# Kernel tuning notes

Measured on AMD Instinct MI355X. Metric: run time of the kernel, lower is better.

Reference implementation:

```python
import jax, jax.numpy as jnp
import numpy as np

N_ATOMS = 200000   # total atoms across batch of molecules
N_BONDS = 400000   # total directed bonds
HSIZE   = 256      # mpn_size
MLP     = 512      # mlp_size
BS_OUT  = 5        # bond edit classes (bs_outdim)
N_MOLS  = 1000     # batch of molecules (len(atom_scope))


def _p(k, shape, scale):
    return jax.random.normal(k, shape, jnp.float32) * scale


def setup_inputs() -> dict:
    key = jax.random.key(0)
    ks = jax.random.split(key, 12)
    s_h = 1.0 / np.sqrt(HSIZE).astype(np.float32)
    s_2h = 1.0 / np.sqrt(2 * HSIZE).astype(np.float32)
    s_m = 1.0 / np.sqrt(MLP).astype(np.float32)
    return {
        'c_atom':  jax.random.normal(ks[0], (N_ATOMS, HSIZE), jnp.float32),
        'ha_prev': jax.random.normal(ks[1], (N_ATOMS, HSIZE), jnp.float32),
        'W_vv':    jnp.eye(HSIZE, dtype=jnp.float32),  # nn.init.eye_ in original
        'W_vc':    _p(ks[2], (HSIZE, HSIZE), s_h),
        'bond_W1': _p(ks[3], (2 * HSIZE, MLP), s_2h),
        'bond_b1': jnp.zeros((MLP,), jnp.float32),
        'bond_W2': _p(ks[4], (MLP, BS_OUT), s_m),
        'bond_b2': jnp.zeros((BS_OUT,), jnp.float32),
        'uni_W1':  _p(ks[5], (HSIZE, MLP), s_h),
        'uni_b1':  jnp.zeros((MLP,), jnp.float32),
        'uni_W2':  _p(ks[6], (MLP, 1), s_m),
        'uni_b2':  jnp.zeros((1,), jnp.float32),
        'done_W1': _p(ks[7], (HSIZE, MLP), s_h),
        'done_b1': jnp.zeros((MLP,), jnp.float32),
        'done_W2': _p(ks[8], (MLP, 1), s_m),
        'done_b2': jnp.zeros((1,), jnp.float32),
        'mol_id':     jax.random.randint(ks[9], (N_ATOMS,), 0, N_MOLS, jnp.int32),
        'bond_index': jax.random.randint(ks[10], (N_BONDS, 2), 0, N_ATOMS, jnp.int32),
    }


def _mlp(x, W1, b1, W2, b2):
    # build_mlp: Linear -> ReLU -> (dropout, off at eval) -> Linear
    return jax.nn.relu(x @ W1 + b1) @ W2 + b2


def reference(c_atom, ha_prev, W_vv, W_vc,
              bond_W1, bond_b1, bond_W2, bond_b2,
              uni_W1, uni_b1, uni_W2, uni_b2,
              done_W1, done_b1, done_W2, done_b2,
              mol_id, bond_index):
    # ha = relu(W_vv @ ha_prev + W_vc @ c_atom); ha[0] = 0 (padding atom)
    ha = jax.nn.relu(ha_prev @ W_vv + c_atom @ W_vc)
    ha = ha.at[0].set(0.0)
    # per-molecule pooling (replaces python loop over atom_scope)
    hm = jax.ops.segment_sum(ha, mol_id, num_segments=N_MOLS)  # [N_MOLS, H]
    # gather bond endpoint embeddings (index_select_ND)
    bond_in = jnp.concatenate([ha[bond_index[:, 0]], ha[bond_index[:, 1]]], axis=-1)  # [E, 2H]
    bond_logits = _mlp(bond_in, bond_W1, bond_b1, bond_W2, bond_b2)  # [E, BS_OUT]
    uni_logits = _mlp(ha, uni_W1, uni_b1, uni_W2, uni_b2)            # [N, 1]
    done_logits = _mlp(hm, done_W1, done_b1, done_W2, done_b2)       # [M, 1]
    # edit_logits in original is a ragged per-mol concat of these three;
    # return the dense flat concatenation (same values, fixed shape)
    return jnp.concatenate([bond_logits.ravel(), uni_logits.ravel(), done_logits.ravel()])
```

## Files before the change

### kernel.cpp

```cpp
#include <hip/hip_runtime.h>
#include <hip/hip_bf16.h>

typedef __attribute__((ext_vector_type(8))) short bf16x8;
typedef __attribute__((ext_vector_type(4))) float f32x4;

static __device__ __forceinline__ unsigned short f2bf(float f) {
    union { float f; unsigned u; } v; v.f = f;
    unsigned r = v.u + 0x7fffu + ((v.u >> 16) & 1u);
    return (unsigned short)(r >> 16);
}

#define GLOAD16(g, l) __builtin_amdgcn_global_load_lds( \
    (const __attribute__((address_space(1))) void*)(g), \
    (__attribute__((address_space(3))) void*)(l), 16, 0, 0)

__global__ __launch_bounds__(256) void conv_weights(
    const float* __restrict__ Wvv, const float* __restrict__ Wvc,
    const float* __restrict__ bW1, const float* __restrict__ uW1,
    unsigned short* __restrict__ WcT, unsigned short* __restrict__ bW1T,
    unsigned short* __restrict__ uW1T)
{
    int idx = blockIdx.x * 256 + threadIdx.x;
    if (idx < 131072) {
        int n = idx & 255, k = idx >> 8;
        float s = (k < 256) ? Wvv[k * 256 + n] : Wvc[(k - 256) * 256 + n];
        WcT[((k >> 3) * 256 + n) * 8 + (k & 7)] = f2bf(s);
    } else if (idx < 131072 + 262144) {
        int t = idx - 131072;
        int n = t & 511, k = t >> 9;
        bW1T[((k >> 3) * 512 + n) * 8 + (k & 7)] = f2bf(bW1[k * 512 + n]);
    } else if (idx < 131072 + 262144 + 131072) {
        int t = idx - 393216;
        int n = t & 511, k = t >> 9;
        uW1T[((k >> 3) * 512 + n) * 8 + (k & 7)] = f2bf(uW1[k * 512 + n]);
    }
}

__global__ __launch_bounds__(512, 4) void ha_kernel(
    const float* __restrict__ ha_prev, const float* __restrict__ c_atom,
    const unsigned short* __restrict__ WcT, const int* __restrict__ mol_id,
    unsigned short* __restrict__ haB, float* __restrict__ hm, int NA)
{
    __shared__ __align__(16) unsigned short As[2][128 * 64];

    const int tid = threadIdx.x;
    const int wv = tid >> 6, lane = tid & 63;
    const int wr = wv >> 2, wc = wv & 3;
    const int c15 = lane & 15, kq = lane >> 4;
    const int xm3 = (c15 & 7) << 3;
    const int m0 = blockIdx.x * 128;

    const int cr0 = tid >> 3, chc = tid & 7;
    const int cr1 = (512 + tid) >> 3;
    int row0 = m0 + cr0; if (row0 >= NA) row0 = NA - 1;
    int row1 = m0 + cr1; if (row1 >= NA) row1 = NA - 1;

    f32x4 v00, v01, v10, v11;
    #define HA_LOAD(ks) { \
        const float* src = ((ks) < 4) ? ha_prev : c_atom; \
        const int kb = ((ks) & 3) * 64 + chc * 8; \
        const float* s0 = src + (size_t)row0 * 256 + kb; \
        const float* s1 = src + (size_t)row1 * 256 + kb; \
        v00 = *(const f32x4*)s0; v01 = *(const f32x4*)(s0 + 4); \
        v10 = *(const f32x4*)s1; v11 = *(const f32x4*)(s1 + 4); }
    #define HA_WRITE(buf) { \
        bf16x8 p0, p1; \
        p0[0]=(short)f2bf(v00[0]); p0[1]=(short)f2bf(v00[1]); p0[2]=(short)f2bf(v00[2]); p0[3]=(short)f2bf(v00[3]); \
        p0[4]=(short)f2bf(v01[0]); p0[5]=(short)f2bf(v01[1]); p0[6]=(short)f2bf(v01[2]); p0[7]=(short)f2bf(v01[3]); \
        p1[0]=(short)f2bf(v10[0]); p1[1]=(short)f2bf(v10[1]); p1[2]=(short)f2bf(v10[2]); p1[3]=(short)f2bf(v10[3]); \
        p1[4]=(short)f2bf(v11[0]); p1[5]=(short)f2bf(v11[1]); p1[6]=(short)f2bf(v11[2]); p1[7]=(short)f2bf(v11[3]); \
        *(bf16x8*)&As[buf][cr0 * 64 + ((chc * 8) ^ ((cr0 & 7) << 3))] = p0; \
        *(bf16x8*)&As[buf][cr1 * 64 + ((chc * 8) ^ ((cr1 & 7) << 3))] = p1; }

    f32x4 acc[4][4];
#pragma unroll
    for (int m = 0; m < 4; ++m)
#pragma unroll
        for (int n = 0; n < 4; ++n) acc[m][n] = (f32x4){0.f, 0.f, 0.f, 0.f};

    HA_LOAD(0); HA_WRITE(0);
    __syncthreads();

    for (int ks = 0; ks < 8; ++ks) {
        if (ks < 7) HA_LOAD(ks + 1);
        const int buf = ks & 1;
#pragma unroll
        for (int kk = 0; kk < 2; ++kk) {
            bf16x8 aF[4], bF[4];
            const int plane = ks * 8 + kk * 4 + kq;
#pragma unroll
            for (int n = 0; n < 4; ++n)
                bF[n] = *(const bf16x8*)(WcT + ((size_t)plane * 256 + wc * 64 + n * 16 + c15) * 8);
#pragma unroll
            for (int m = 0; m < 4; ++m)
                aF[m] = *(const bf16x8*)&As[buf][(wr * 64 + m * 16 + c15) * 64 + ((kk * 32 + kq * 8) ^ xm3)];
#pragma unroll
            for (int m = 0; m < 4; ++m)
#pragma unroll
                for (int n = 0; n < 4; ++n)
                    acc[m][n] = __builtin_amdgcn_mfma_f32_16x16x32_bf16(aF[m], bF[n], acc[m][n], 0, 0, 0);
        }
        if (ks < 7) HA_WRITE((ks + 1) & 1);
        __syncthreads();
    }

#pragma unroll
    for (int m = 0; m < 4; ++m) {
#pragma unroll
        for (int reg = 0; reg < 4; ++reg) {
            int row = m0 + wr * 64 + m * 16 + kq * 4 + reg;
            if (row >= NA) continue;
            bool z = (row == 0);
            int mol = z ? 0 : mol_id[row];
#pragma unroll
            for (int n = 0; n < 4; ++n) {
                int col = wc * 64 + n * 16 + c15;
                float v = fmaxf(acc[m][n][reg], 0.f);
                if (z) v = 0.f;
                haB[(size_t)row * 256 + col] = f2bf(v);
                if (!z) atomicAdd(&hm[mol * 256 + col], v);
            }
        }
    }
}

__global__ __launch_bounds__(512, 4) void bond_kernel(
    const unsigned short* __restrict__ haB, const int* __restrict__ bidx,
    const unsigned short* __restrict__ bW1T, const float* __restrict__ b1,
    const float* __restrict__ W2, const float* __restrict__ b2,
    float* __restrict__ outB, int NB)
{
    __shared__ __align__(16) unsigned short As[64 * 512];
    __shared__ float obuf[64][5];

    const int tid = threadIdx.x;
    const int wv = tid >> 6, lane = tid & 63;
    const int c15 = lane & 15, kq = lane >> 4;
    const int b0 = blockIdx.x * 64;

    if (tid < 320) ((float*)obuf)[tid] = 0.f;

    const int ep = lane >> 5, sl = lane & 31;
    int eidx[8];
#pragma unroll
    for (int i = 0; i < 8; ++i) {
        int gb = b0 + wv * 8 + i; if (gb >= NB) gb = 0;
        eidx[i] = bidx[gb * 2 + ep];
    }
#pragma unroll
    for (int i = 0; i < 8; ++i) {
        int r = wv * 8 + i;
        GLOAD16(haB + (size_t)eidx[i] * 256 + (size_t)((sl ^ (r & 7)) * 8),
                As + r * 512);
    }
    __syncthreads();

    f32x4 acc[4][4];
#pragma unroll
    for (int m = 0; m < 4; ++m)
#pragma unroll
        for (int n = 0; n < 4; ++n) acc[m][n] = (f32x4){0.f, 0.f, 0.f, 0.f};

    for (int ks = 0; ks < 8; ++ks) {
#pragma unroll
        for (int kk = 0; kk < 2; ++kk) {
            bf16x8 aF[4], bF[4];
            const int plane = ks * 8 + kk * 4 + kq;
#pragma unroll
            for (int n = 0; n < 4; ++n)
                bF[n] = *(const bf16x8*)(bW1T + ((size_t)plane * 512 + wv * 64 + n * 16 + c15) * 8);
#pragma unroll
            for (int m = 0; m < 4; ++m) {
                int r = m * 16 + c15;
                int ch = (((ks & 3) * 8 + kk * 4 + kq) ^ (r & 7));
                aF[m] = *(const bf16x8*)&As[r * 512 + (ks >> 2) * 256 + ch * 8];
            }
#pragma unroll
            for (int m = 0; m < 4; ++m)
#pragma unroll
                for (int n = 0; n < 4; ++n)
                    acc[m][n] = __builtin_amdgcn_mfma_f32_16x16x32_bf16(aF[m], bF[n], acc[m][n], 0, 0, 0);
        }
    }

    float b1c[4], w2c[4][5];
#pragma unroll
    for (int n = 0; n < 4; ++n) {
        int col = wv * 64 + n * 16 + c15;
        b1c[n] = b1[col];
#pragma unroll
        for (int j = 0; j < 5; ++j) w2c[n][j] = W2[col * 5 + j];
    }
#pragma unroll
    for (int m = 0; m < 4; ++m) {
#pragma unroll
        for (int reg = 0; reg < 4; ++reg) {
            float s[5] = {0.f, 0.f, 0.f, 0.f, 0.f};
#pragma unroll
            for (int n = 0; n < 4; ++n) {
                float p = fmaxf(acc[m][n][reg] + b1c[n], 0.f);
#pragma unroll
                for (int j = 0; j < 5; ++j) s[j] += p * w2c[n][j];
            }
#pragma unroll
            for (int off = 1; off < 16; off <<= 1)
#pragma unroll
                for (int j = 0; j < 5; ++j) s[j] += __shfl_xor(s[j], off);
            if (c15 == 0) {
                int rl = m * 16 + kq * 4 + reg;
#pragma unroll
                for (int j = 0; j < 5; ++j) atomicAdd(&obuf[rl][j], s[j]);
            }
        }
    }
    __syncthreads();
    {
        int r = tid >> 3, j = tid & 7;
        if (j < 5) {
            int row = b0 + r;
            if (row < NB) outB[(size_t)row * 5 + j] = obuf[r][j] + b2[j];
        }
    }
}

__global__ __launch_bounds__(512, 4) void uni_kernel(
    const unsigned short* __restrict__ haB, const unsigned short* __restrict__ uW1T,
    const float* __restrict__ b1, const float* __restrict__ W2,
    const float* __restrict__ b2, float* __restrict__ outU, int NA)
{
    __shared__ __align__(16) unsigned short As[64 * 256];
    __shared__ float obuf[64];

    const int tid = threadIdx.x;
    const int wv = tid >> 6, lane = tid & 63;
    const int c15 = lane & 15, kq = lane >> 4;
    const int a0 = blockIdx.x * 64;

    if (tid < 64) obuf[tid] = 0.f;

    const int rr = lane >> 5, sl = lane & 31;
#pragma unroll
    for (int i = 0; i < 4; ++i) {
        int r = wv * 8 + i * 2 + rr;
        int ga = a0 + r; if (ga >= NA) ga = NA - 1;
        GLOAD16(haB + (size_t)ga * 256 + (size_t)((sl ^ (r & 7)) * 8),
                As + (wv * 8 + i * 2) * 256);
    }
    __syncthreads();

    f32x4 acc[4][4];
#pragma unroll
    for (int m = 0; m < 4; ++m)
#pragma unroll
        for (int n = 0; n < 4; ++n) acc[m][n] = (f32x4){0.f, 0.f, 0.f, 0.f};

    for (int ks = 0; ks < 4; ++ks) {
#pragma unroll
        for (int kk = 0; kk < 2; ++kk) {
            bf16x8 aF[4], bF[4];
            const int plane = ks * 8 + kk * 4 + kq;
#pragma unroll
            for (int n = 0; n < 4; ++n)
                bF[n] = *(const bf16x8*)(uW1T + ((size_t)plane * 512 + wv * 64 + n * 16 + c15) * 8);
#pragma unroll
            for (int m = 0; m < 4; ++m) {
                int r = m * 16 + c15;
                int ch = ((ks * 8 + kk * 4 + kq) ^ (r & 7));
                aF[m] = *(const bf16x8*)&As[r * 256 + ch * 8];
            }
#pragma unroll
            for (int m = 0; m < 4; ++m)
#pragma unroll
                for (int n = 0; n < 4; ++n)
                    acc[m][n] = __builtin_amdgcn_mfma_f32_16x16x32_bf16(aF[m], bF[n], acc[m][n], 0, 0, 0);
        }
    }

    float b1c[4], w2c[4];
#pragma unroll
    for (int n = 0; n < 4; ++n) {
        int col = wv * 64 + n * 16 + c15;
        b1c[n] = b1[col];
        w2c[n] = W2[col];
    }
#pragma unroll
    for (int m = 0; m < 4; ++m) {
#pragma unroll
        for (int reg = 0; reg < 4; ++reg) {
            float s = 0.f;
#pragma unroll
            for (int n = 0; n < 4; ++n)
                s += fmaxf(acc[m][n][reg] + b1c[n], 0.f) * w2c[n];
#pragma unroll
            for (int off = 1; off < 16; off <<= 1) s += __shfl_xor(s, off);
            if (c15 == 0) atomicAdd(&obuf[m * 16 + kq * 4 + reg], s);
        }
    }
    __syncthreads();
    if (tid < 64) {
        int row = a0 + tid;
        if (row < NA) outU[row] = obuf[tid] + b2[0];
    }
}

__global__ __launch_bounds__(256) void done_kernel(
    const float* __restrict__ hm, const float* __restrict__ W1,
    const float* __restrict__ b1, const float* __restrict__ W2,
    const float* __restrict__ b2, float* __restrict__ outD, int NM)
{
    __shared__ float rsh[4][256];
    __shared__ float red[4][4];
    const int tid = threadIdx.x;
    const int wv = tid >> 6, lane = tid & 63;
    const int mol0 = blockIdx.x * 4;
#pragma unroll
    for (int q = 0; q < 4; ++q)
        rsh[q][tid] = (mol0 + q < NM) ? hm[(size_t)(mol0 + q) * 256 + tid] : 0.f;
    __syncthreads();
    float h[4][2];
#pragma unroll
    for (int q = 0; q < 4; ++q) { h[q][0] = 0.f; h[q][1] = 0.f; }
    for (int k = 0; k < 256; ++k) {
        float w0 = W1[k * 512 + tid];
        float w1 = W1[k * 512 + tid + 256];
#pragma unroll
        for (int q = 0; q < 4; ++q) {
            h[q][0] += rsh[q][k] * w0;
            h[q][1] += rsh[q][k] * w1;
        }
    }
    float bb0 = b1[tid], bb1v = b1[tid + 256];
    float ww0 = W2[tid], ww1 = W2[tid + 256];
#pragma unroll
    for (int q = 0; q < 4; ++q) {
        float p = fmaxf(h[q][0] + bb0, 0.f) * ww0 + fmaxf(h[q][1] + bb1v, 0.f) * ww1;
#pragma unroll
        for (int off = 1; off < 64; off <<= 1) p += __shfl_xor(p, off);
        if (lane == 0) red[q][wv] = p;
    }
    __syncthreads();
    if (tid < 4 && mol0 + tid < NM)
        outD[mol0 + tid] = red[tid][0] + red[tid][1] + red[tid][2] + red[tid][3] + b2[0];
}

extern "C" void kernel_launch(void* const* d_in, const int* in_sizes, int n_in,
                              void* d_out, int out_size, void* d_ws, size_t ws_size,
                              hipStream_t stream)
{
    const float* c_atom  = (const float*)d_in[0];
    const float* ha_prev = (const float*)d_in[1];
    const float* W_vv    = (const float*)d_in[2];
    const float* W_vc    = (const float*)d_in[3];
    const float* bW1     = (const float*)d_in[4];
    const float* bb1     = (const float*)d_in[5];
    const float* bW2     = (const float*)d_in[6];
    const float* bb2     = (const float*)d_in[7];
    const float* uW1     = (const float*)d_in[8];
    const float* ub1     = (const float*)d_in[9];
    const float* uW2     = (const float*)d_in[10];
    const float* ub2     = (const float*)d_in[11];
    const float* dW1     = (const float*)d_in[12];
    const float* db1     = (const float*)d_in[13];
    const float* dW2     = (const float*)d_in[14];
    const float* db2     = (const float*)d_in[15];
    const int* mol_id    = (const int*)d_in[16];
    const int* bidx      = (const int*)d_in[17];

    const int H = 256, BS = 5;
    const int NA = in_sizes[0] / H;
    const int NB = in_sizes[17] / 2;
    const int NM = out_size - NB * BS - NA;

    float* out  = (float*)d_out;
    float* outB = out;
    float* outU = out + (size_t)NB * BS;
    float* outD = outU + NA;

    char* ws = (char*)d_ws;
    size_t off = 0;
    unsigned short* haB = (unsigned short*)(ws + off);
    off += (size_t)NA * H * 2;            off = (off + 255) & ~(size_t)255;
    float* hm = (float*)(ws + off);
    off += (size_t)NM * H * 4;            off = (off + 255) & ~(size_t)255;
    unsigned short* WcT = (unsigned short*)(ws + off);
    off += (size_t)131072 * 2;            off = (off + 255) & ~(size_t)255;
    unsigned short* bW1T = (unsigned short*)(ws + off);
    off += (size_t)262144 * 2;            off = (off + 255) & ~(size_t)255;
    unsigned short* uW1T = (unsigned short*)(ws + off);

    hipMemsetAsync(hm, 0, (size_t)NM * H * 4, stream);
    conv_weights<<<2048, 256, 0, stream>>>(W_vv, W_vc, bW1, uW1, WcT, bW1T, uW1T);
    ha_kernel<<<(NA + 127) / 128, 512, 0, stream>>>(ha_prev, c_atom, WcT, mol_id, haB, hm, NA);
    bond_kernel<<<(NB + 63) / 64, 512, 0, stream>>>(haB, bidx, bW1T, bb1, bW2, bb2, outB, NB);
    uni_kernel<<<(NA + 63) / 64, 512, 0, stream>>>(haB, uW1T, ub1, uW2, ub2, outU, NA);
    done_kernel<<<(NM + 3) / 4, 256, 0, stream>>>(hm, dW1, db1, dW2, db2, outD, NM);
}
```

Baseline: 633.3 us.

## Retile LDS A staging by K-blocks and double-buffer weight fragment loads

The bond and uni kernels now stage the gathered activation tile in LDS as 64-column K-blocks, with each wave loading one K-slab across all rows instead of whole rows. The MFMA loop is fully unrolled and prefetches the next step's weight fragments into a second register buffer while the current step computes. The intent is to hide global weight-load latency behind the MFMAs and to change the gather access pattern. The extra register buffer may reduce occupancy under the launch bound.

```diff
diff --git a/kernel.cpp b/kernel.cpp
--- a/kernel.cpp
+++ b/kernel.cpp
@@ -130,7 +130,7 @@
     const float* __restrict__ W2, const float* __restrict__ b2,
     float* __restrict__ outB, int NB)
 {
-    __shared__ __align__(16) unsigned short As[64 * 512];
+    __shared__ __align__(16) unsigned short As[8 * 64 * 64];
     __shared__ float obuf[64][5];
 
     const int tid = threadIdx.x;
@@ -140,18 +140,21 @@
 
     if (tid < 320) ((float*)obuf)[tid] = 0.f;
 
-    const int ep = lane >> 5, sl = lane & 31;
-    int eidx[8];
-#pragma unroll
-    for (int i = 0; i < 8; ++i) {
-        int gb = b0 + wv * 8 + i; if (gb >= NB) gb = 0;
-        eidx[i] = bidx[gb * 2 + ep];
-    }
-#pragma unroll
-    for (int i = 0; i < 8; ++i) {
-        int r = wv * 8 + i;
-        GLOAD16(haB + (size_t)eidx[i] * 256 + (size_t)((sl ^ (r & 7)) * 8),
-                As + r * 512);
+    {
+        const int ep = wv >> 2, koff = (wv & 3) * 64;
+        const int rsub = lane >> 3, csub = lane & 7;
+        int eidxs[8];
+#pragma unroll
+        for (int j = 0; j < 8; ++j) {
+            int gb = b0 + j * 8 + rsub; if (gb >= NB) gb = 0;
+            eidxs[j] = bidx[gb * 2 + ep];
+        }
+#pragma unroll
+        for (int j = 0; j < 8; ++j) {
+            int r = j * 8 + rsub;
+            GLOAD16(haB + (size_t)eidxs[j] * 256 + koff + (size_t)((csub ^ (r & 7)) * 8),
+                    As + wv * 4096 + j * 512);
+        }
     }
     __syncthreads();
 
@@ -161,26 +164,33 @@
 #pragma unroll
         for (int n = 0; n < 4; ++n) acc[m][n] = (f32x4){0.f, 0.f, 0.f, 0.f};
 
-    for (int ks = 0; ks < 8; ++ks) {
-#pragma unroll
-        for (int kk = 0; kk < 2; ++kk) {
-            bf16x8 aF[4], bF[4];
-            const int plane = ks * 8 + kk * 4 + kq;
-#pragma unroll
-            for (int n = 0; n < 4; ++n)
-                bF[n] = *(const bf16x8*)(bW1T + ((size_t)plane * 512 + wv * 64 + n * 16 + c15) * 8);
-#pragma unroll
-            for (int m = 0; m < 4; ++m) {
-                int r = m * 16 + c15;
-                int ch = (((ks & 3) * 8 + kk * 4 + kq) ^ (r & 7));
-                aF[m] = *(const bf16x8*)&As[r * 512 + (ks >> 2) * 256 + ch * 8];
-            }
-#pragma unroll
-            for (int m = 0; m < 4; ++m)
-#pragma unroll
-                for (int n = 0; n < 4; ++n)
-                    acc[m][n] = __builtin_amdgcn_mfma_f32_16x16x32_bf16(aF[m], bF[n], acc[m][n], 0, 0, 0);
-        }
+    bf16x8 breg[2][4];
+    {
+        const int pl0 = kq;
+#pragma unroll
+        for (int n = 0; n < 4; ++n)
+            breg[0][n] = *(const bf16x8*)(bW1T + ((size_t)pl0 * 512 + wv * 64 + n * 16 + c15) * 8);
+    }
+#pragma unroll
+    for (int s = 0; s < 16; ++s) {
+        if (s < 15) {
+            const int pl = ((s + 1) >> 1) * 8 + ((s + 1) & 1) * 4 + kq;
+#pragma unroll
+            for (int n = 0; n < 4; ++n)
+                breg[(s + 1) & 1][n] = *(const bf16x8*)(bW1T + ((size_t)pl * 512 + wv * 64 + n * 16 + c15) * 8);
+        }
+        const int ks = s >> 1, kk = s & 1;
+        bf16x8 aF[4];
+#pragma unroll
+        for (int m = 0; m < 4; ++m) {
+            int r = m * 16 + c15;
+            aF[m] = *(const bf16x8*)&As[ks * 4096 + r * 64 + (((kk * 4 + kq) ^ (r & 7)) * 8)];
+        }
+#pragma unroll
+        for (int m = 0; m < 4; ++m)
+#pragma unroll
+            for (int n = 0; n < 4; ++n)
+                acc[m][n] = __builtin_amdgcn_mfma_f32_16x16x32_bf16(aF[m], breg[s & 1][n], acc[m][n], 0, 0, 0);
     }
 
     float b1c[4], w2c[4][5];
@@ -228,7 +238,7 @@
     const float* __restrict__ b1, const float* __restrict__ W2,
     const float* __restrict__ b2, float* __restrict__ outU, int NA)
 {
-    __shared__ __align__(16) unsigned short As[64 * 256];
+    __shared__ __align__(16) unsigned short As[4 * 64 * 64];
     __shared__ float obuf[64];
 
     const int tid = threadIdx.x;
@@ -238,13 +248,17 @@
 
     if (tid < 64) obuf[tid] = 0.f;
 
-    const int rr = lane >> 5, sl = lane & 31;
-#pragma unroll
-    for (int i = 0; i < 4; ++i) {
-        int r = wv * 8 + i * 2 + rr;
-        int ga = a0 + r; if (ga >= NA) ga = NA - 1;
-        GLOAD16(haB + (size_t)ga * 256 + (size_t)((sl ^ (r & 7)) * 8),
-                As + (wv * 8 + i * 2) * 256);
+    {
+        const int kt = wv >> 1, koff = kt * 64;
+        const int rsub = lane >> 3, csub = lane & 7;
+#pragma unroll
+        for (int jj = 0; jj < 4; ++jj) {
+            int j = (wv & 1) * 4 + jj;
+            int r = j * 8 + rsub;
+            int ga = a0 + r; if (ga >= NA) ga = NA - 1;
+            GLOAD16(haB + (size_t)ga * 256 + koff + (size_t)((csub ^ (r & 7)) * 8),
+                    As + kt * 4096 + j * 512);
+        }
     }
     __syncthreads();
 
@@ -254,26 +268,33 @@
 #pragma unroll
         for (int n = 0; n < 4; ++n) acc[m][n] = (f32x4){0.f, 0.f, 0.f, 0.f};
 
-    for (int ks = 0; ks < 4; ++ks) {
-#pragma unroll
-        for (int kk = 0; kk < 2; ++kk) {
-            bf16x8 aF[4], bF[4];
-            const int plane = ks * 8 + kk * 4 + kq;
-#pragma unroll
-            for (int n = 0; n < 4; ++n)
-                bF[n] = *(const bf16x8*)(uW1T + ((size_t)plane * 512 + wv * 64 + n * 16 + c15) * 8);
-#pragma unroll
-            for (int m = 0; m < 4; ++m) {
-                int r = m * 16 + c15;
-                int ch = ((ks * 8 + kk * 4 + kq) ^ (r & 7));
-                aF[m] = *(const bf16x8*)&As[r * 256 + ch * 8];
-            }
-#pragma unroll
-            for (int m = 0; m < 4; ++m)
-#pragma unroll
-                for (int n = 0; n < 4; ++n)
-                    acc[m][n] = __builtin_amdgcn_mfma_f32_16x16x32_bf16(aF[m], bF[n], acc[m][n], 0, 0, 0);
-        }
+    bf16x8 breg[2][4];
+    {
+        const int pl0 = kq;
+#pragma unroll
+        for (int n = 0; n < 4; ++n)
+            breg[0][n] = *(const bf16x8*)(uW1T + ((size_t)pl0 * 512 + wv * 64 + n * 16 + c15) * 8);
+    }
+#pragma unroll
+    for (int s = 0; s < 8; ++s) {
+        if (s < 7) {
+            const int pl = ((s + 1) >> 1) * 8 + ((s + 1) & 1) * 4 + kq;
+#pragma unroll
+            for (int n = 0; n < 4; ++n)
+                breg[(s + 1) & 1][n] = *(const bf16x8*)(uW1T + ((size_t)pl * 512 + wv * 64 + n * 16 + c15) * 8);
+        }
+        const int ks = s >> 1, kk = s & 1;
+        bf16x8 aF[4];
+#pragma unroll
+        for (int m = 0; m < 4; ++m) {
+            int r = m * 16 + c15;
+            aF[m] = *(const bf16x8*)&As[ks * 4096 + r * 64 + (((kk * 4 + kq) ^ (r & 7)) * 8)];
+        }
+#pragma unroll
+        for (int m = 0; m < 4; ++m)
+#pragma unroll
+            for (int n = 0; n < 4; ++n)
+                acc[m][n] = __builtin_amdgcn_mfma_f32_16x16x32_bf16(aF[m], breg[s & 1][n], acc[m][n], 0, 0, 0);
     }
 
     float b1c[4], w2c[4];
```

Measured after the change: 650.9 us. 2.8% more time.
